# Kernel optimization log

Hardware: AMD Instinct MI355X
Metric: run time of the kernel (lower is better)

## Reference

```python
import jax, jax.numpy as jnp
import numpy as np

D_MODEL = 1024
NUM_HEADS = 16
HEAD_DIM = D_MODEL // NUM_HEADS
ROPE_THETA = 10000.0


def apply_rope(x, positions):
    # x: (B, H, S, Dh), positions: (S,) int
    half = x.shape[-1] // 2
    inv_freq = ROPE_THETA ** (-jnp.arange(half, dtype=jnp.float32) * 2.0 / x.shape[-1])  # (Dh/2,)
    ang = positions.astype(jnp.float32)[:, None] * inv_freq[None, :]  # (S, Dh/2)
    cos, sin = jnp.cos(ang), jnp.sin(ang)
    x1 = x[..., 0::2]  # (B,H,S,Dh/2)
    x2 = x[..., 1::2]
    r1 = x1 * cos - x2 * sin
    r2 = x1 * sin + x2 * cos
    return jnp.stack([r1, r2], axis=-1).reshape(x.shape)


def setup_inputs() -> dict:
    key = jax.random.key(0)
    ks = jax.random.split(key, 5)
    B, S = 2, 2048
    scale = 1.0 / np.sqrt(D_MODEL)
    x = jax.random.normal(ks[0], (B, S, D_MODEL), dtype=jnp.float32)
    Wq = jax.random.normal(ks[1], (D_MODEL, D_MODEL), dtype=jnp.float32) * scale
    Wk = jax.random.normal(ks[2], (D_MODEL, D_MODEL), dtype=jnp.float32) * scale
    Wv = jax.random.normal(ks[3], (D_MODEL, D_MODEL), dtype=jnp.float32) * scale
    Wo = jax.random.normal(ks[4], (D_MODEL, D_MODEL), dtype=jnp.float32) * scale
    token_positions = jnp.arange(S, dtype=jnp.int32)
    return {"x": x, "token_positions": token_positions, "Wq": Wq, "Wk": Wk, "Wv": Wv, "Wo": Wo}


def reference(x, token_positions, Wq, Wk, Wv, Wo):
    B, S, _ = x.shape
    # Linear is bias-free: y = x @ W.T (W: [out, in])
    def proj(W):
        y = jnp.einsum('bsd,ed->bse', x, W)
        return y.reshape(B, S, NUM_HEADS, HEAD_DIM).transpose(0, 2, 1, 3)  # (B,H,S,Dh)
    q, k, v = proj(Wq), proj(Wk), proj(Wv)
    q = apply_rope(q, token_positions)
    k = apply_rope(k, token_positions)
    scores = jnp.einsum('bhqd,bhkd->bhqk', q, k) / jnp.sqrt(jnp.float32(HEAD_DIM))
    causal = jnp.tril(jnp.ones((S, S), dtype=bool))
    scores = jnp.where(causal, scores, -jnp.inf)
    attn = jax.nn.softmax(scores, axis=-1)
    out = jnp.einsum('bhqk,bhkd->bhqd', attn, v)  # (B,H,S,Dh)
    out = out.transpose(0, 2, 1, 3).reshape(B, S, D_MODEL)
    return jnp.einsum('bsd,ed->bse', out, Wo)
```

## Files before the change

### kernel.cpp

```cpp
#include <hip/hip_runtime.h>


typedef unsigned short u16;
typedef unsigned int   u32;
typedef unsigned long long u64;
using s16x8 = __attribute__((ext_vector_type(8))) short;
using f32x4 = __attribute__((ext_vector_type(4))) float;

__device__ __forceinline__ u16 f2bf(float f) {
  union { float f; u32 u; } v; v.f = f;
  return (u16)((v.u + 0x7fffu + ((v.u >> 16) & 1u)) >> 16);
}
__device__ __forceinline__ float bf2f(u16 h) {
  union { u32 u; float f; } v; v.u = ((u32)h) << 16;
  return v.f;
}

__device__ __forceinline__ void gl2lds(const u16* g, u16* l) {
  __builtin_amdgcn_global_load_lds(
      (const __attribute__((address_space(1))) void*)g,
      (__attribute__((address_space(3))) void*)l, 16, 0, 0);
}

__global__ __launch_bounds__(256) void cvt_all(
    const float* __restrict__ x,
    const float* __restrict__ wq, const float* __restrict__ wk,
    const float* __restrict__ wv, const float* __restrict__ wo,
    u16* __restrict__ xb, u16* __restrict__ wqb, u16* __restrict__ wkb,
    u16* __restrict__ wvb, u16* __restrict__ wob) {
  int e = (blockIdx.x * 256 + threadIdx.x) * 4;
  const float* src; u16* dst; int off;
  const int XN = 4 << 20;
  if (e < XN) { src = x; dst = xb; off = e; }
  else {
    int t = e - XN; int sel = t >> 20; off = t & ((1 << 20) - 1);
    src = sel == 0 ? wq : sel == 1 ? wk : sel == 2 ? wv : wo;
    dst = sel == 0 ? wqb : sel == 1 ? wkb : sel == 2 ? wvb : wob;
  }
  float4 v = *(const float4*)(src + off);
  ushort4 o;
  o.x = f2bf(v.x); o.y = f2bf(v.y); o.z = f2bf(v.z); o.w = f2bf(v.w);
  *(ushort4*)(dst + off) = o;
}

__device__ __forceinline__ void gemm_core(
    const u16* __restrict__ A, const u16* __restrict__ W,
    u16* As, u16* Bs, int bm0, int bn0, f32x4 (&acc)[4][4]) {
  const int K = 1024;
  int tid = threadIdx.x;
  int wid = tid >> 6, lane = tid & 63, quad = lane >> 4, l15 = lane & 15;
  int wm = (wid >> 1) * 64, wn = (wid & 1) * 64;
  int ch0 = wid * 128 + lane, ch1 = ch0 + 64;
  int r0 = ch0 >> 2, c0 = (ch0 & 3) * 8;
  int r1 = ch1 >> 2, c1 = (ch1 & 3) * 8;
  const u16* Ab = A + (size_t)bm0 * K;
  const u16* Wb = W + (size_t)bn0 * K;
  u16* lA0 = As + wid * 1024; u16* lA1 = lA0 + 512;
  u16* lB0 = Bs + wid * 1024; u16* lB1 = lB0 + 512;
  for (int k0 = 0; k0 < K; k0 += 32) {
    __syncthreads();
    gl2lds(Ab + (size_t)r0 * K + k0 + c0, lA0);
    gl2lds(Ab + (size_t)r1 * K + k0 + c1, lA1);
    gl2lds(Wb + (size_t)r0 * K + k0 + c0, lB0);
    gl2lds(Wb + (size_t)r1 * K + k0 + c1, lB1);
    __syncthreads();
    s16x8 af[4], bf[4];
#pragma unroll
    for (int mi = 0; mi < 4; mi++)
      af[mi] = *(const s16x8*)(As + (wm + mi * 16 + l15) * 32 + quad * 8);
#pragma unroll
    for (int ni = 0; ni < 4; ni++)
      bf[ni] = *(const s16x8*)(Bs + (wn + ni * 16 + l15) * 32 + quad * 8);
#pragma unroll
    for (int mi = 0; mi < 4; mi++)
#pragma unroll
      for (int ni = 0; ni < 4; ni++)
        acc[mi][ni] = __builtin_amdgcn_mfma_f32_16x16x32_bf16(
            af[mi], bf[ni], acc[mi][ni], 0, 0, 0);
  }
}

__global__ __launch_bounds__(256) void gemm_qkv(
    const u16* __restrict__ xb,
    const u16* __restrict__ wq, const u16* __restrict__ wk,
    const u16* __restrict__ wv, const int* __restrict__ pos,
    u16* __restrict__ qh, u16* __restrict__ kh, u16* __restrict__ vt) {
  __shared__ __align__(16) u16 As[128 * 32];
  __shared__ __align__(16) u16 Bs[128 * 32];
  __shared__ __align__(16) float tab[128 * 32 * 2];
  int z = blockIdx.z;
  const u16* W = (z == 0) ? wq : (z == 1) ? wk : wv;
  int bm0 = blockIdx.y * 128, bn0 = blockIdx.x * 128;
  int tid = threadIdx.x;
  if (z < 2) {
    for (int idx = tid; idx < 4096; idx += 256) {
      int rl = idx >> 5, pair = idx & 31;
      int s = (bm0 + rl) & 2047;
      float p = (float)pos[s];
      float freq = __expf(-0.28782313662425572f * (float)pair);
      float sn, cs;
      sincosf(p * freq, &sn, &cs);
      tab[idx * 2] = cs;
      tab[idx * 2 + 1] = sn;
    }
  }
  f32x4 acc[4][4];
  const f32x4 fz = {0.f, 0.f, 0.f, 0.f};
#pragma unroll
  for (int mi = 0; mi < 4; mi++)
#pragma unroll
    for (int ni = 0; ni < 4; ni++) acc[mi][ni] = fz;
  gemm_core(xb, W, As, Bs, bm0, bn0, acc);
  int wid = tid >> 6, lane = tid & 63;
  int quad = lane >> 4, l15 = lane & 15;
  int wm = (wid >> 1) * 64, wn = (wid & 1) * 64;
  if (z < 2) {
    u16* dst = (z == 0) ? qh : kh;
    float qs = (z == 0) ? 0.125f : 1.0f;
#pragma unroll
    for (int mi = 0; mi < 4; mi++)
#pragma unroll
      for (int ni = 0; ni < 4; ni++) {
        int col = bn0 + wn + ni * 16 + l15;
        int h = col >> 6, d = col & 63;
        int pairi = d >> 1;
        int odd = d & 1;
#pragma unroll
        for (int r = 0; r < 4; r++) {
          int rl = wm + mi * 16 + quad * 4 + r;
          int row = bm0 + rl;
          int b = row >> 11, s = row & 2047;
          float v0 = acc[mi][ni][r];
          float vp = __shfl_xor(v0, 1, 64);
          float cs = tab[(rl * 32 + pairi) * 2];
          float sn = tab[(rl * 32 + pairi) * 2 + 1];
          float o = odd ? (vp * sn + v0 * cs) : (v0 * cs - vp * sn);
          dst[(((size_t)(b * 16 + h)) * 2048 + s) * 64 + d] = f2bf(o * qs);
        }
      }
  } else {
#pragma unroll
    for (int mi = 0; mi < 4; mi++)
#pragma unroll
      for (int ni = 0; ni < 4; ni++) {
        int row0 = bm0 + wm + mi * 16 + quad * 4;
        int col = bn0 + wn + ni * 16 + l15;
        int b = row0 >> 11, s0 = row0 & 2047, h = col >> 6, d = col & 63;
        u64 pk = (u64)f2bf(acc[mi][ni][0]) |
                 ((u64)f2bf(acc[mi][ni][1]) << 16) |
                 ((u64)f2bf(acc[mi][ni][2]) << 32) |
                 ((u64)f2bf(acc[mi][ni][3]) << 48);
        *(u64*)(vt + (((size_t)(b * 16 + h)) * 64 + d) * 2048 + s0) = pk;
      }
  }
}

__global__ __launch_bounds__(256) void gemm_out(
    const u16* __restrict__ ao, const u16* __restrict__ wo,
    float* __restrict__ out) {
  __shared__ __align__(16) u16 As[128 * 32];
  __shared__ __align__(16) u16 Bs[128 * 32];
  int bm0 = blockIdx.y * 128, bn0 = blockIdx.x * 128;
  f32x4 acc[4][4];
  const f32x4 fz = {0.f, 0.f, 0.f, 0.f};
#pragma unroll
  for (int mi = 0; mi < 4; mi++)
#pragma unroll
    for (int ni = 0; ni < 4; ni++) acc[mi][ni] = fz;
  gemm_core(ao, wo, As, Bs, bm0, bn0, acc);
  int tid = threadIdx.x, wid = tid >> 6, lane = tid & 63;
  int quad = lane >> 4, l15 = lane & 15;
  int wm = (wid >> 1) * 64, wn = (wid & 1) * 64;
#pragma unroll
  for (int mi = 0; mi < 4; mi++)
#pragma unroll
    for (int ni = 0; ni < 4; ni++)
#pragma unroll
      for (int r = 0; r < 4; r++) {
        int row = bm0 + wm + mi * 16 + quad * 4 + r;
        int col = bn0 + wn + ni * 16 + l15;
        out[(size_t)row * 1024 + col] = acc[mi][ni][r];
      }
}

#define KTS 72
#define VTS 72
#define PTS 40
#define OTS 72

__global__ __launch_bounds__(256, 4) void attn_k(
    const u16* __restrict__ qh, const u16* __restrict__ kh,
    const u16* __restrict__ vt, u16* __restrict__ ao) {
  __shared__ __align__(16) u16 ks[64 * KTS];
  __shared__ __align__(16) u16 vs[64 * VTS];
  __shared__ __align__(16) u16 pt[4 * 16 * PTS];
  int bid = blockIdx.x;
  int bh = bid & 31, pi = bid >> 5;
  int b = bh >> 4, h = bh & 15;
  int tid = threadIdx.x, wid = tid >> 6, lane = tid & 63;
  int quad = lane >> 4, l15 = lane & 15;
  int qsub = wid & 1, thalf = wid >> 1;
  const u16* qbase = qh + (size_t)bh * 2048 * 64;
  const u16* kbase = kh + (size_t)bh * 2048 * 64;
  const u16* vbase = vt + (size_t)bh * 64 * 2048;
  u16* ptw = pt + wid * 16 * PTS;
  const f32x4 fz = {0.f, 0.f, 0.f, 0.f};
  int srow = tid >> 2, sc = (tid & 3) * 8;

#pragma unroll
  for (int phase = 0; phase < 2; phase++) {
    int qt = phase ? (63 - pi) : pi;
    int q0 = qt * 32, q0w = q0 + qsub * 16;
    s16x8 qf0 = *(const s16x8*)(qbase + (size_t)(q0w + l15) * 64 + quad * 8);
    s16x8 qf1 = *(const s16x8*)(qbase + (size_t)(q0w + l15) * 64 + 32 + quad * 8);
    f32x4 acc[4];
#pragma unroll
    for (int md = 0; md < 4; md++) acc[md] = fz;
    float lsum = 0.f;
    int qg = q0w + l15;
    int nt = (qt >> 1) + 1;
    uint4 rk0 = *(const uint4*)(kbase + (size_t)srow * 64 + sc);
    uint4 rk1 = *(const uint4*)(kbase + (size_t)srow * 64 + sc + 32);
    uint4 rv0 = *(const uint4*)(vbase + (size_t)srow * 2048 + sc);
    uint4 rv1 = *(const uint4*)(vbase + (size_t)srow * 2048 + sc + 32);
    for (int it = 0; it < nt; it++) {
      __syncthreads();
      *(uint4*)(ks + srow * KTS + sc) = rk0;
      *(uint4*)(ks + srow * KTS + sc + 32) = rk1;
      *(uint4*)(vs + srow * VTS + sc) = rv0;
      *(uint4*)(vs + srow * VTS + sc + 32) = rv1;
      if (it + 1 < nt) {
        int t1 = (it + 1) << 6;
        rk0 = *(const uint4*)(kbase + (size_t)(t1 + srow) * 64 + sc);
        rk1 = *(const uint4*)(kbase + (size_t)(t1 + srow) * 64 + sc + 32);
        rv0 = *(const uint4*)(vbase + (size_t)srow * 2048 + t1 + sc);
        rv1 = *(const uint4*)(vbase + (size_t)srow * 2048 + t1 + sc + 32);
      }
      __syncthreads();
      int t0 = it << 6, tb = thalf * 32;
      bool diag = (it == nt - 1);
#pragma unroll
      for (int mt = 0; mt < 2; mt++) {
        int krow = tb + mt * 16 + l15;
        s16x8 ka0 = *(const s16x8*)(ks + krow * KTS + quad * 8);
        s16x8 ka1 = *(const s16x8*)(ks + krow * KTS + 32 + quad * 8);
        f32x4 st = __builtin_amdgcn_mfma_f32_16x16x32_bf16(ka0, qf0, fz, 0, 0, 0);
        st = __builtin_amdgcn_mfma_f32_16x16x32_bf16(ka1, qf1, st, 0, 0, 0);
        u64 pk = 0;
#pragma unroll
        for (int r = 0; r < 4; r++) {
          float p = __expf(st[r]);
          if (diag) {
            int tg = t0 + tb + mt * 16 + quad * 4 + r;
            if (tg > qg) p = 0.f;
          }
          lsum += p;
          pk |= ((u64)f2bf(p)) << (16 * r);
        }
        *(u64*)(ptw + l15 * PTS + mt * 16 + quad * 4) = pk;
      }
      s16x8 pb = *(const s16x8*)(ptw + l15 * PTS + quad * 8);
#pragma unroll
      for (int md = 0; md < 4; md++) {
        s16x8 va = *(const s16x8*)(vs + (md * 16 + l15) * VTS + tb + quad * 8);
        acc[md] = __builtin_amdgcn_mfma_f32_16x16x32_bf16(va, pb, acc[md], 0, 0, 0);
      }
    }
    lsum += __shfl_xor(lsum, 16, 64);
    lsum += __shfl_xor(lsum, 32, 64);
    __syncthreads();
    float* redo = (float*)ks;
    float* redl = (float*)vs;
    if (thalf == 1) {
#pragma unroll
      for (int md = 0; md < 4; md++)
#pragma unroll
        for (int r = 0; r < 4; r++)
          redo[(qsub * 64 + lane) * 16 + md * 4 + r] = acc[md][r];
      redl[qsub * 64 + lane] = lsum;
    }
    __syncthreads();
    if (thalf == 0) {
#pragma unroll
      for (int md = 0; md < 4; md++)
#pragma unroll
        for (int r = 0; r < 4; r++)
          acc[md][r] += redo[(qsub * 64 + lane) * 16 + md * 4 + r];
      lsum += redl[qsub * 64 + lane];
      float rl = 1.0f / lsum;
      u16* ow = pt + qsub * 16 * OTS;
#pragma unroll
      for (int md = 0; md < 4; md++) {
        u64 ok = 0;
#pragma unroll
        for (int r = 0; r < 4; r++)
          ok |= ((u64)f2bf(acc[md][r] * rl)) << (16 * r);
        *(u64*)(ow + l15 * OTS + md * 16 + quad * 4) = ok;
      }
      int qq = lane >> 2, dc = lane & 3;
      uint4 o0 = *(uint4*)(ow + qq * OTS + dc * 16);
      uint4 o1 = *(uint4*)(ow + qq * OTS + dc * 16 + 8);
      size_t orow = (size_t)b * 2048 + q0 + qsub * 16 + qq;
      *(uint4*)(ao + orow * 1024 + h * 64 + dc * 16) = o0;
      *(uint4*)(ao + orow * 1024 + h * 64 + dc * 16 + 8) = o1;
    }
  }
}

extern "C" void kernel_launch(void* const* d_in, const int* in_sizes, int n_in,
                              void* d_out, int out_size, void* d_ws,
                              size_t ws_size, hipStream_t stream) {
  const float* x  = (const float*)d_in[0];
  const int* pos  = (const int*)d_in[1];
  const float* Wq = (const float*)d_in[2];
  const float* Wk = (const float*)d_in[3];
  const float* Wv = (const float*)d_in[4];
  const float* Wo = (const float*)d_in[5];
  float* out = (float*)d_out;

  char* ws = (char*)d_ws;
  const size_t MB = 1u << 20;
  u16* xb  = (u16*)(ws);
  u16* wqb = (u16*)(ws + 8 * MB);
  u16* wkb = (u16*)(ws + 10 * MB);
  u16* wvb = (u16*)(ws + 12 * MB);
  u16* wob = (u16*)(ws + 14 * MB);
  u16* qhb = (u16*)(ws + 16 * MB);
  u16* khb = (u16*)(ws + 24 * MB);
  u16* vtb = (u16*)(ws + 32 * MB);
  u16* ao  = xb;

  cvt_all<<<8192, 256, 0, stream>>>(x, Wq, Wk, Wv, Wo,
                                    xb, wqb, wkb, wvb, wob);
  gemm_qkv<<<dim3(8, 32, 3), 256, 0, stream>>>(xb, wqb, wkb, wvb, pos,
                                               qhb, khb, vtb);
  attn_k<<<1024, 256, 0, stream>>>(qhb, khb, vtb, ao);
  gemm_out<<<dim3(8, 32), 256, 0, stream>>>(ao, wob, out);
}
```

Baseline: 210.6 us.

## Precompute RoPE table in convert kernel and split-K the output projection

The RoPE cos/sin table is now computed once for all 2048 positions by extra blocks in the conversion kernel and read from global memory in the QKV GEMM epilogue. Before, every Q/K block recomputed its own slice into shared memory. The output projection GEMM is split into two K halves, launching 512 blocks instead of 256 to fill the GPU's compute units better, and a separate kernel adds the two fp32 partials. Split-K costs an extra 32 MB of partial-buffer traffic and one more launch, and both paths depend on the workspace being large enough.

```diff
diff --git a/kernel.cpp b/kernel.cpp
--- a/kernel.cpp
+++ b/kernel.cpp
@@ -27,8 +27,20 @@
     const float* __restrict__ wq, const float* __restrict__ wk,
     const float* __restrict__ wv, const float* __restrict__ wo,
     u16* __restrict__ xb, u16* __restrict__ wqb, u16* __restrict__ wkb,
-    u16* __restrict__ wvb, u16* __restrict__ wob) {
-  int e = (blockIdx.x * 256 + threadIdx.x) * 4;
+    u16* __restrict__ wvb, u16* __restrict__ wob,
+    float* __restrict__ rtab, const int* __restrict__ pos) {
+  int bid = blockIdx.x;
+  if (bid >= 8192) {
+    int idx = (bid - 8192) * 256 + threadIdx.x;
+    int s = idx >> 5, pair = idx & 31;
+    float p = (float)pos[s];
+    float freq = __expf(-0.28782313662425572f * (float)pair);
+    float sn, cs;
+    sincosf(p * freq, &sn, &cs);
+    *(float2*)(rtab + idx * 2) = make_float2(cs, sn);
+    return;
+  }
+  int e = (bid * 256 + threadIdx.x) * 4;
   const float* src; u16* dst; int off;
   const int XN = 4 << 20;
   if (e < XN) { src = x; dst = xb; off = e; }
@@ -45,7 +57,7 @@
 
 __device__ __forceinline__ void gemm_core(
     const u16* __restrict__ A, const u16* __restrict__ W,
-    u16* As, u16* Bs, int bm0, int bn0, f32x4 (&acc)[4][4]) {
+    u16* As, u16* Bs, int bm0, int bn0, int kb, int ke, f32x4 (&acc)[4][4]) {
   const int K = 1024;
   int tid = threadIdx.x;
   int wid = tid >> 6, lane = tid & 63, quad = lane >> 4, l15 = lane & 15;
@@ -57,7 +69,7 @@
   const u16* Wb = W + (size_t)bn0 * K;
   u16* lA0 = As + wid * 1024; u16* lA1 = lA0 + 512;
   u16* lB0 = Bs + wid * 1024; u16* lB1 = lB0 + 512;
-  for (int k0 = 0; k0 < K; k0 += 32) {
+  for (int k0 = kb; k0 < ke; k0 += 32) {
     __syncthreads();
     gl2lds(Ab + (size_t)r0 * K + k0 + c0, lA0);
     gl2lds(Ab + (size_t)r1 * K + k0 + c1, lA1);
@@ -80,19 +92,21 @@
   }
 }
 
-__global__ __launch_bounds__(256) void gemm_qkv(
+template <bool TAB>
+__global__ __launch_bounds__(256) void gemm_qkv_t(
     const u16* __restrict__ xb,
     const u16* __restrict__ wq, const u16* __restrict__ wk,
     const u16* __restrict__ wv, const int* __restrict__ pos,
+    const float* __restrict__ rtab,
     u16* __restrict__ qh, u16* __restrict__ kh, u16* __restrict__ vt) {
   __shared__ __align__(16) u16 As[128 * 32];
   __shared__ __align__(16) u16 Bs[128 * 32];
-  __shared__ __align__(16) float tab[128 * 32 * 2];
+  __shared__ __align__(16) float tabl[TAB ? 2 : 128 * 32 * 2];
   int z = blockIdx.z;
   const u16* W = (z == 0) ? wq : (z == 1) ? wk : wv;
   int bm0 = blockIdx.y * 128, bn0 = blockIdx.x * 128;
   int tid = threadIdx.x;
-  if (z < 2) {
+  if (!TAB && z < 2) {
     for (int idx = tid; idx < 4096; idx += 256) {
       int rl = idx >> 5, pair = idx & 31;
       int s = (bm0 + rl) & 2047;
@@ -100,8 +114,8 @@
       float freq = __expf(-0.28782313662425572f * (float)pair);
       float sn, cs;
       sincosf(p * freq, &sn, &cs);
-      tab[idx * 2] = cs;
-      tab[idx * 2 + 1] = sn;
+      tabl[idx * 2] = cs;
+      tabl[idx * 2 + 1] = sn;
     }
   }
   f32x4 acc[4][4];
@@ -110,7 +124,7 @@
   for (int mi = 0; mi < 4; mi++)
 #pragma unroll
     for (int ni = 0; ni < 4; ni++) acc[mi][ni] = fz;
-  gemm_core(xb, W, As, Bs, bm0, bn0, acc);
+  gemm_core(xb, W, As, Bs, bm0, bn0, 0, 1024, acc);
   int wid = tid >> 6, lane = tid & 63;
   int quad = lane >> 4, l15 = lane & 15;
   int wm = (wid >> 1) * 64, wn = (wid & 1) * 64;
@@ -132,8 +146,14 @@
           int b = row >> 11, s = row & 2047;
           float v0 = acc[mi][ni][r];
           float vp = __shfl_xor(v0, 1, 64);
-          float cs = tab[(rl * 32 + pairi) * 2];
-          float sn = tab[(rl * 32 + pairi) * 2 + 1];
+          float cs, sn;
+          if (TAB) {
+            float2 t = *(const float2*)(rtab + (size_t)(s * 32 + pairi) * 2);
+            cs = t.x; sn = t.y;
+          } else {
+            cs = tabl[(rl * 32 + pairi) * 2];
+            sn = tabl[(rl * 32 + pairi) * 2 + 1];
+          }
           float o = odd ? (vp * sn + v0 * cs) : (v0 * cs - vp * sn);
           dst[(((size_t)(b * 16 + h)) * 2048 + s) * 64 + d] = f2bf(o * qs);
         }
@@ -155,6 +175,46 @@
   }
 }
 
+__global__ __launch_bounds__(256) void gemm_out_sk(
+    const u16* __restrict__ ao, const u16* __restrict__ wo,
+    float* __restrict__ pbuf) {
+  __shared__ __align__(16) u16 As[128 * 32];
+  __shared__ __align__(16) u16 Bs[128 * 32];
+  int bm0 = blockIdx.y * 128, bn0 = blockIdx.x * 128;
+  int kb = blockIdx.z * 512;
+  f32x4 acc[4][4];
+  const f32x4 fz = {0.f, 0.f, 0.f, 0.f};
+#pragma unroll
+  for (int mi = 0; mi < 4; mi++)
+#pragma unroll
+    for (int ni = 0; ni < 4; ni++) acc[mi][ni] = fz;
+  gemm_core(ao, wo, As, Bs, bm0, bn0, kb, kb + 512, acc);
+  int tid = threadIdx.x, wid = tid >> 6, lane = tid & 63;
+  int quad = lane >> 4, l15 = lane & 15;
+  int wm = (wid >> 1) * 64, wn = (wid & 1) * 64;
+  float* dst = pbuf + (size_t)blockIdx.z * (4u << 20);
+#pragma unroll
+  for (int mi = 0; mi < 4; mi++)
+#pragma unroll
+    for (int ni = 0; ni < 4; ni++)
+#pragma unroll
+      for (int r = 0; r < 4; r++) {
+        int row = bm0 + wm + mi * 16 + quad * 4 + r;
+        int col = bn0 + wn + ni * 16 + l15;
+        dst[(size_t)row * 1024 + col] = acc[mi][ni][r];
+      }
+}
+
+__global__ __launch_bounds__(256) void add_out(
+    const float* __restrict__ p, float* __restrict__ o) {
+  int i = (blockIdx.x * 256 + threadIdx.x) * 4;
+  float4 a = *(const float4*)(p + i);
+  float4 b = *(const float4*)(p + (4u << 20) + i);
+  float4 r;
+  r.x = a.x + b.x; r.y = a.y + b.y; r.z = a.z + b.z; r.w = a.w + b.w;
+  *(float4*)(o + i) = r;
+}
+
 __global__ __launch_bounds__(256) void gemm_out(
     const u16* __restrict__ ao, const u16* __restrict__ wo,
     float* __restrict__ out) {
@@ -167,7 +227,7 @@
   for (int mi = 0; mi < 4; mi++)
 #pragma unroll
     for (int ni = 0; ni < 4; ni++) acc[mi][ni] = fz;
-  gemm_core(ao, wo, As, Bs, bm0, bn0, acc);
+  gemm_core(ao, wo, As, Bs, bm0, bn0, 0, 1024, acc);
   int tid = threadIdx.x, wid = tid >> 6, lane = tid & 63;
   int quad = lane >> 4, l15 = lane & 15;
   int wm = (wid >> 1) * 64, wn = (wid & 1) * 64;
@@ -328,12 +388,26 @@
   u16* qhb = (u16*)(ws + 16 * MB);
   u16* khb = (u16*)(ws + 24 * MB);
   u16* vtb = (u16*)(ws + 32 * MB);
+  float* rtab = (float*)(ws + 40 * MB);
+  float* pbuf = (float*)(ws + 41 * MB);
   u16* ao  = xb;
 
-  cvt_all<<<8192, 256, 0, stream>>>(x, Wq, Wk, Wv, Wo,
-                                    xb, wqb, wkb, wvb, wob);
-  gemm_qkv<<<dim3(8, 32, 3), 256, 0, stream>>>(xb, wqb, wkb, wvb, pos,
-                                               qhb, khb, vtb);
+  bool tabok = ws_size >= 41 * MB;
+  bool skok  = ws_size >= 73 * MB;
+
+  cvt_all<<<tabok ? 8448 : 8192, 256, 0, stream>>>(
+      x, Wq, Wk, Wv, Wo, xb, wqb, wkb, wvb, wob, rtab, pos);
+  if (tabok)
+    gemm_qkv_t<true><<<dim3(8, 32, 3), 256, 0, stream>>>(
+        xb, wqb, wkb, wvb, pos, rtab, qhb, khb, vtb);
+  else
+    gemm_qkv_t<false><<<dim3(8, 32, 3), 256, 0, stream>>>(
+        xb, wqb, wkb, wvb, pos, rtab, qhb, khb, vtb);
   attn_k<<<1024, 256, 0, stream>>>(qhb, khb, vtb, ao);
-  gemm_out<<<dim3(8, 32), 256, 0, stream>>>(ao, wob, out);
-}
+  if (skok) {
+    gemm_out_sk<<<dim3(8, 32, 2), 256, 0, stream>>>(ao, wob, pbuf);
+    add_out<<<4096, 256, 0, stream>>>(pbuf, out);
+  } else {
+    gemm_out<<<dim3(8, 32), 256, 0, stream>>>(ao, wob, out);
+  }
+}
```

After: 207.5 us. About the same (-1.5%).
